# Kernel optimization log

Measured on AMD Instinct MI355X. Metric: run time of the kernel, lower is better.

Reference implementation:

```python
import jax, jax.numpy as jnp
import numpy as np

EMBED = 128
HEADS = 4
HEAD_DIM = EMBED // HEADS

def setup_inputs() -> dict:
    key = jax.random.key(0)
    ks = jax.random.split(key, 8)
    N, S = 32, 1024
    values = jax.random.normal(ks[0], (N, S, EMBED), dtype=jnp.float32)
    keys_ = jax.random.normal(ks[1], (N, S, EMBED), dtype=jnp.float32)
    query = jax.random.normal(ks[2], (N, S, EMBED), dtype=jnp.float32)
    mask = jnp.ones((N, 1, S, S), dtype=jnp.int32)
    # nn.Linear weights: y = x @ W.T  (bias=False for q/k/v projections)
    sc = 1.0 / np.sqrt(HEAD_DIM)
    Wv = jax.random.uniform(ks[3], (HEAD_DIM, HEAD_DIM), jnp.float32, -sc, sc)
    Wk = jax.random.uniform(ks[4], (HEAD_DIM, HEAD_DIM), jnp.float32, -sc, sc)
    Wq = jax.random.uniform(ks[5], (HEAD_DIM, HEAD_DIM), jnp.float32, -sc, sc)
    so = 1.0 / np.sqrt(EMBED)
    Wo = jax.random.uniform(ks[6], (EMBED, EMBED), jnp.float32, -so, so)
    bo = jax.random.uniform(ks[7], (EMBED,), jnp.float32, -so, so)
    return {"values": values, "keys": keys_, "query": query, "mask": mask,
            "Wv": Wv, "Wk": Wk, "Wq": Wq, "Wo": Wo, "bo": bo}

def reference(values, keys, query, mask, Wv, Wk, Wq, Wo, bo):
    N = query.shape[0]
    # reshape to [N, S, H, D] and apply per-head linear projections (no bias)
    v = values.reshape(N, -1, HEADS, HEAD_DIM) @ Wv.T
    k = keys.reshape(N, -1, HEADS, HEAD_DIM) @ Wk.T
    q = query.reshape(N, -1, HEADS, HEAD_DIM) @ Wq.T
    # [N, H, Sq, Sk]
    att = jnp.einsum('nqhd,nkhd->nhqk', q, k)
    att = jnp.where(mask == 0, jnp.float32(-1e20), att)
    # NOTE: faithful to source: scale by sqrt(embed_size), not sqrt(head_dim)
    attention_weights = jax.nn.softmax(att / jnp.sqrt(jnp.float32(EMBED)), axis=3)
    out = jnp.einsum('nhql,nlhd->nqhd', attention_weights, v).reshape(N, -1, HEADS * HEAD_DIM)
    out = out @ Wo.T + bo
    return out, attention_weights
```

## Files before the change

### kernel.cpp

```cpp
#include <hip/hip_runtime.h>

#define SLEN 1024
#define NBATCH 32
#define NHEADS 4
#define HDIM 32
#define EMB 128
#define LSTRIDE 1040

typedef short short8 __attribute__((ext_vector_type(8)));
typedef short short4v __attribute__((ext_vector_type(4)));
typedef float floatx4 __attribute__((ext_vector_type(4)));

__device__ __forceinline__ unsigned short f2bf(float f) {
    unsigned u = __float_as_uint(f);
    u += 0x7fffu + ((u >> 16) & 1u);
    return (unsigned short)(u >> 16);
}
__device__ __forceinline__ float bf2f(unsigned short h) {
    return __uint_as_float(((unsigned)h) << 16);
}

__global__ __launch_bounds__(256) void proj_kernel(
    const float* __restrict__ vals, const float* __restrict__ keys,
    const float* __restrict__ qrys,
    const float* __restrict__ Wv, const float* __restrict__ Wk,
    const float* __restrict__ Wq, const float* __restrict__ Wo,
    unsigned short* __restrict__ qb, unsigned short* __restrict__ kb,
    unsigned short* __restrict__ vt, unsigned short* __restrict__ wo_bf)
{
    int b = blockIdx.x;
    int tid = threadIdx.x;
    if (b == 512) {
        #pragma unroll
        for (int i = 0; i < 64; ++i) {
            int idx = tid + (i << 8);
            wo_bf[idx] = f2bf(Wo[idx]);
        }
        return;
    }
    int n = b >> 4;
    int s0 = (b & 15) << 6;
    int wave = tid >> 6, lane = tid & 63;
    int quad = lane >> 4, l16 = lane & 15;
    int srow = s0 + (wave << 4);

    short8 bw[3][2];
    const float* Ws[3] = { Wv, Wk, Wq };
    const float scal[3] = { 1.0f, 1.0f, 0.08838834764831845f };
    #pragma unroll
    for (int t = 0; t < 3; ++t) {
        float s = scal[t];
        #pragma unroll
        for (int hh = 0; hh < 2; ++hh) {
            const float* wp = Ws[t] + (hh * 16 + l16) * 32 + quad * 8;
            float4 w0 = *(const float4*)wp;
            float4 w1 = *(const float4*)(wp + 4);
            short8 r;
            r[0] = (short)f2bf(w0.x * s); r[1] = (short)f2bf(w0.y * s);
            r[2] = (short)f2bf(w0.z * s); r[3] = (short)f2bf(w0.w * s);
            r[4] = (short)f2bf(w1.x * s); r[5] = (short)f2bf(w1.y * s);
            r[6] = (short)f2bf(w1.z * s); r[7] = (short)f2bf(w1.w * s);
            bw[t][hh] = r;
        }
    }

    const float* srcs[3] = { vals, keys, qrys };
    #pragma unroll
    for (int t = 0; t < 3; ++t) {
        const float* src = srcs[t];
        #pragma unroll
        for (int h = 0; h < NHEADS; ++h) {
            size_t nh = (size_t)(n * NHEADS + h);
            const float* xp = src + ((size_t)(n * SLEN + srow + l16) * EMB + h * HDIM + quad * 8);
            float4 x0 = *(const float4*)xp;
            float4 x1 = *(const float4*)(xp + 4);
            short8 a;
            a[0] = (short)f2bf(x0.x); a[1] = (short)f2bf(x0.y);
            a[2] = (short)f2bf(x0.z); a[3] = (short)f2bf(x0.w);
            a[4] = (short)f2bf(x1.x); a[5] = (short)f2bf(x1.y);
            a[6] = (short)f2bf(x1.z); a[7] = (short)f2bf(x1.w);
            floatx4 c0 = {0.f, 0.f, 0.f, 0.f};
            floatx4 c1 = {0.f, 0.f, 0.f, 0.f};
            c0 = __builtin_amdgcn_mfma_f32_16x16x32_bf16(a, bw[t][0], c0, 0, 0, 0);
            c1 = __builtin_amdgcn_mfma_f32_16x16x32_bf16(a, bw[t][1], c1, 0, 0, 0);
            if (t == 0) {
                short4v p0, p1;
                p0[0] = (short)f2bf(c0[0]); p0[1] = (short)f2bf(c0[1]);
                p0[2] = (short)f2bf(c0[2]); p0[3] = (short)f2bf(c0[3]);
                p1[0] = (short)f2bf(c1[0]); p1[1] = (short)f2bf(c1[1]);
                p1[2] = (short)f2bf(c1[2]); p1[3] = (short)f2bf(c1[3]);
                *(short4v*)(vt + (nh * HDIM + l16) * SLEN + srow + quad * 4) = p0;
                *(short4v*)(vt + (nh * HDIM + 16 + l16) * SLEN + srow + quad * 4) = p1;
            } else {
                unsigned short* dst = (t == 1 ? kb : qb) +
                    (nh * SLEN + srow + quad * 4) * HDIM;
                #pragma unroll
                for (int r = 0; r < 4; ++r) {
                    dst[r * HDIM + l16]      = f2bf(c0[r]);
                    dst[r * HDIM + 16 + l16] = f2bf(c1[r]);
                }
            }
        }
    }
}

__global__ __launch_bounds__(256, 3) void attn_kernel(
    const unsigned short* __restrict__ qb, const unsigned short* __restrict__ kb,
    const unsigned short* __restrict__ vt, const int* __restrict__ mask,
    float* __restrict__ wout, unsigned short* __restrict__ attnv)
{
    __shared__ unsigned short eb[16 * LSTRIDE];
    __shared__ float partial[4][16][32];
    __shared__ float rowinv[16];

    int bid = blockIdx.x;
    int n = bid >> 6;
    int r0 = (bid & 63) << 4;
    int tid = threadIdx.x;
    int wave = tid >> 6, lane = tid & 63;
    int quad = lane >> 4, l16 = lane & 15;
    int srow = tid >> 4, c16 = tid & 15;

    unsigned long long mbits = 0ull;
    const int* mrow = mask + (size_t)(n * SLEN + r0 + srow) * SLEN;
    #pragma unroll
    for (int i = 0; i < 8; ++i) {
        int cb = (c16 + (i << 4)) << 3;
        int4 a = *(const int4*)(mrow + cb);
        int4 bq = *(const int4*)(mrow + cb + 4);
        unsigned bits = 0;
        bits |= (unsigned)(a.x != 0);
        bits |= (unsigned)(a.y != 0) << 1;
        bits |= (unsigned)(a.z != 0) << 2;
        bits |= (unsigned)(a.w != 0) << 3;
        bits |= (unsigned)(bq.x != 0) << 4;
        bits |= (unsigned)(bq.y != 0) << 5;
        bits |= (unsigned)(bq.z != 0) << 6;
        bits |= (unsigned)(bq.w != 0) << 7;
        mbits |= (unsigned long long)bits << (i * 8);
    }

    for (int h = 0; h < NHEADS; ++h) {
        size_t nh = (size_t)(n * NHEADS + h);

        short8 afrag = *(const short8*)(qb + (nh * SLEN + r0 + l16) * HDIM + quad * 8);
        const unsigned short* kbase = kb + nh * SLEN * HDIM;
        #pragma unroll
        for (int t = 0; t < 16; ++t) {
            int ct = (wave << 4) + t;
            short8 bfrag = *(const short8*)(kbase + (size_t)((ct << 4) + l16) * HDIM + quad * 8);
            floatx4 c = {0.f, 0.f, 0.f, 0.f};
            c = __builtin_amdgcn_mfma_f32_16x16x32_bf16(afrag, bfrag, c, 0, 0, 0);
            int colb = (ct << 4) + l16;
            #pragma unroll
            for (int r = 0; r < 4; ++r)
                eb[(quad * 4 + r) * LSTRIDE + colb] = f2bf(c[r]);
        }
        __syncthreads();

        unsigned short* erow = eb + srow * LSTRIDE;
        float mx = -3.0e38f;
        #pragma unroll
        for (int i = 0; i < 8; ++i) {
            int cb = (c16 + (i << 4)) << 3;
            short8 v = *(const short8*)(erow + cb);
            unsigned bits = (unsigned)(mbits >> (i * 8)) & 0xffu;
            #pragma unroll
            for (int j = 0; j < 8; ++j) {
                float x = ((bits >> j) & 1u) ? bf2f((unsigned short)v[j]) : -1e20f;
                mx = fmaxf(mx, x);
            }
        }
        #pragma unroll
        for (int off = 8; off > 0; off >>= 1)
            mx = fmaxf(mx, __shfl_xor(mx, off, 16));

        float sum = 0.f;
        #pragma unroll
        for (int i = 0; i < 8; ++i) {
            int cb = (c16 + (i << 4)) << 3;
            short8 v = *(const short8*)(erow + cb);
            unsigned bits = (unsigned)(mbits >> (i * 8)) & 0xffu;
            short8 e8;
            #pragma unroll
            for (int j = 0; j < 8; ++j) {
                float e = 0.f;
                if ((bits >> j) & 1u) e = __expf(bf2f((unsigned short)v[j]) - mx);
                sum += e;
                e8[j] = (short)f2bf(e);
            }
            *(short8*)(erow + cb) = e8;
        }
        #pragma unroll
        for (int off = 8; off > 0; off >>= 1)
            sum += __shfl_xor(sum, off, 16);
        float inv = 1.0f / sum;
        if (c16 == 0) rowinv[srow] = inv;

        float* wrow = wout + (nh * SLEN + r0 + srow) * SLEN;
        #pragma unroll
        for (int i = 0; i < 8; ++i) {
            int cb = (c16 + (i << 4)) << 3;
            short8 e8 = *(const short8*)(erow + cb);
            float4 w0, w1;
            w0.x = bf2f((unsigned short)e8[0]) * inv;
            w0.y = bf2f((unsigned short)e8[1]) * inv;
            w0.z = bf2f((unsigned short)e8[2]) * inv;
            w0.w = bf2f((unsigned short)e8[3]) * inv;
            w1.x = bf2f((unsigned short)e8[4]) * inv;
            w1.y = bf2f((unsigned short)e8[5]) * inv;
            w1.z = bf2f((unsigned short)e8[6]) * inv;
            w1.w = bf2f((unsigned short)e8[7]) * inv;
            *(float4*)(wrow + cb) = w0;
            *(float4*)(wrow + cb + 4) = w1;
        }
        __syncthreads();

        floatx4 acc0 = {0.f, 0.f, 0.f, 0.f}, acc1 = {0.f, 0.f, 0.f, 0.f};
        const unsigned short* vbase = vt + nh * HDIM * SLEN;
        #pragma unroll
        for (int i = 0; i < 8; ++i) {
            int kt = (wave << 3) + i;
            short8 a8 = *(const short8*)(eb + l16 * LSTRIDE + (kt << 5) + quad * 8);
            short8 b0 = *(const short8*)(vbase + (size_t)l16 * SLEN + (kt << 5) + quad * 8);
            short8 b1 = *(const short8*)(vbase + (size_t)(16 + l16) * SLEN + (kt << 5) + quad * 8);
            acc0 = __builtin_amdgcn_mfma_f32_16x16x32_bf16(a8, b0, acc0, 0, 0, 0);
            acc1 = __builtin_amdgcn_mfma_f32_16x16x32_bf16(a8, b1, acc1, 0, 0, 0);
        }
        #pragma unroll
        for (int r = 0; r < 4; ++r) {
            partial[wave][quad * 4 + r][l16] = acc0[r];
            partial[wave][quad * 4 + r][16 + l16] = acc1[r];
        }
        __syncthreads();

        {
            int m = tid >> 4;
            int d0 = (tid & 15) << 1;
            float s0 = partial[0][m][d0] + partial[1][m][d0] +
                       partial[2][m][d0] + partial[3][m][d0];
            float s1 = partial[0][m][d0 + 1] + partial[1][m][d0 + 1] +
                       partial[2][m][d0 + 1] + partial[3][m][d0 + 1];
            float iv = rowinv[m];
            unsigned pk = (unsigned)f2bf(s0 * iv) | ((unsigned)f2bf(s1 * iv) << 16);
            *(unsigned*)(attnv + (size_t)(n * SLEN + r0 + m) * EMB + h * HDIM + d0) = pk;
        }
        __syncthreads();
    }
}

__global__ __launch_bounds__(256) void out_kernel(
    const unsigned short* __restrict__ attnv, const unsigned short* __restrict__ wo_bf,
    const float* __restrict__ bo, float* __restrict__ out)
{
    int tid = threadIdx.x;
    int wave = tid >> 6, lane = tid & 63;
    int quad = lane >> 4, l16 = lane & 15;
    int m0 = blockIdx.x * 64 + (wave << 4);

    short8 afr[4];
    const unsigned short* ap = attnv + (size_t)(m0 + l16) * EMB + quad * 8;
    #pragma unroll
    for (int ks = 0; ks < 4; ++ks) afr[ks] = *(const short8*)(ap + ks * 32);

    #pragma unroll
    for (int ct = 0; ct < 8; ++ct) {
        floatx4 c = {0.f, 0.f, 0.f, 0.f};
        const unsigned short* bp = wo_bf + ((ct << 4) + l16) * EMB + quad * 8;
        #pragma unroll
        for (int ks = 0; ks < 4; ++ks) {
            short8 b = *(const short8*)(bp + ks * 32);
            c = __builtin_amdgcn_mfma_f32_16x16x32_bf16(afr[ks], b, c, 0, 0, 0);
        }
        int col = (ct << 4) + l16;
        float bias = bo[col];
        #pragma unroll
        for (int r = 0; r < 4; ++r)
            out[(size_t)(m0 + quad * 4 + r) * EMB + col] = c[r] + bias;
    }
}

extern "C" void kernel_launch(void* const* d_in, const int* in_sizes, int n_in,
                              void* d_out, int out_size, void* d_ws, size_t ws_size,
                              hipStream_t stream)
{
    (void)in_sizes; (void)n_in; (void)out_size; (void)ws_size;
    const float* vals = (const float*)d_in[0];
    const float* keys = (const float*)d_in[1];
    const float* qrys = (const float*)d_in[2];
    const int*   mask = (const int*)d_in[3];
    const float* Wv   = (const float*)d_in[4];
    const float* Wk   = (const float*)d_in[5];
    const float* Wq   = (const float*)d_in[6];
    const float* Wo   = (const float*)d_in[7];
    const float* bo   = (const float*)d_in[8];
    float* out = (float*)d_out;

    const size_t NHS = (size_t)NBATCH * NHEADS * SLEN * HDIM;
    unsigned short* ws = (unsigned short*)d_ws;
    unsigned short* qb    = ws;
    unsigned short* kbuf  = qb + NHS;
    unsigned short* vt    = kbuf + NHS;
    unsigned short* av    = vt + NHS;
    unsigned short* wo_bf = av + (size_t)NBATCH * SLEN * EMB;
    float* wout = out + (size_t)NBATCH * SLEN * EMB;

    hipLaunchKernelGGL(proj_kernel, dim3(513), dim3(256), 0, stream,
                       vals, keys, qrys, Wv, Wk, Wq, Wo, qb, kbuf, vt, wo_bf);
    hipLaunchKernelGGL(attn_kernel, dim3(NBATCH * 64), dim3(256), 0, stream,
                       qb, kbuf, vt, mask, wout, av);
    hipLaunchKernelGGL(out_kernel, dim3((NBATCH * SLEN) / 64), dim3(256), 0, stream,
                       av, wo_bf, bo, out);
}
```

Measured before the change: 848.4 us.

## Keep QK scores in registers for softmax and use nontemporal stores

The QK^T MFMA is transposed (K as A operand) so each lane holds four consecutive columns of a row. Masking, max, exp and normalisation are then done directly on register accumulators instead of round-tripping bf16 scores through LDS. Row max and sum are reduced across waves through small shared arrays. The mask is repacked once per block into per-lane nibbles via shared memory. The attention-weight, attnv and output writes use nontemporal stores, and one trailing barrier is dropped. The cost is higher register pressure from holding 16 accumulators per lane, and the weights are now computed from fp32 scores rather than bf16-rounded ones.

```diff
diff --git a/kernel.cpp b/kernel.cpp
--- a/kernel.cpp
+++ b/kernel.cpp
@@ -5,11 +5,12 @@
 #define NHEADS 4
 #define HDIM 32
 #define EMB 128
-#define LSTRIDE 1040
+#define LSTRIDE 1032
 
 typedef short short8 __attribute__((ext_vector_type(8)));
 typedef short short4v __attribute__((ext_vector_type(4)));
 typedef float floatx4 __attribute__((ext_vector_type(4)));
+typedef int   intx4  __attribute__((ext_vector_type(4)));
 
 __device__ __forceinline__ unsigned short f2bf(float f) {
     unsigned u = __float_as_uint(f);
@@ -110,8 +111,10 @@
     float* __restrict__ wout, unsigned short* __restrict__ attnv)
 {
     __shared__ unsigned short eb[16 * LSTRIDE];
+    __shared__ unsigned long long mb[16][17];
     __shared__ float partial[4][16][32];
-    __shared__ float rowinv[16];
+    __shared__ __align__(16) float redmax[16][4];
+    __shared__ __align__(16) float redsum[16][4];
 
     int bid = blockIdx.x;
     int n = bid >> 6;
@@ -121,109 +124,116 @@
     int quad = lane >> 4, l16 = lane & 15;
     int srow = tid >> 4, c16 = tid & 15;
 
-    unsigned long long mbits = 0ull;
-    const int* mrow = mask + (size_t)(n * SLEN + r0 + srow) * SLEN;
-    #pragma unroll
-    for (int i = 0; i < 8; ++i) {
-        int cb = (c16 + (i << 4)) << 3;
-        int4 a = *(const int4*)(mrow + cb);
-        int4 bq = *(const int4*)(mrow + cb + 4);
-        unsigned bits = 0;
-        bits |= (unsigned)(a.x != 0);
-        bits |= (unsigned)(a.y != 0) << 1;
-        bits |= (unsigned)(a.z != 0) << 2;
-        bits |= (unsigned)(a.w != 0) << 3;
-        bits |= (unsigned)(bq.x != 0) << 4;
-        bits |= (unsigned)(bq.y != 0) << 5;
-        bits |= (unsigned)(bq.z != 0) << 6;
-        bits |= (unsigned)(bq.w != 0) << 7;
-        mbits |= (unsigned long long)bits << (i * 8);
+    {
+        unsigned long long mbits = 0ull;
+        const int* mrow = mask + (size_t)(n * SLEN + r0 + srow) * SLEN;
+        #pragma unroll
+        for (int i = 0; i < 8; ++i) {
+            int cb = (c16 + (i << 4)) << 3;
+            intx4 a  = __builtin_nontemporal_load((const intx4*)(mrow + cb));
+            intx4 bq = __builtin_nontemporal_load((const intx4*)(mrow + cb + 4));
+            unsigned bits = 0;
+            bits |= (unsigned)(a[0] != 0);
+            bits |= (unsigned)(a[1] != 0) << 1;
+            bits |= (unsigned)(a[2] != 0) << 2;
+            bits |= (unsigned)(a[3] != 0) << 3;
+            bits |= (unsigned)(bq[0] != 0) << 4;
+            bits |= (unsigned)(bq[1] != 0) << 5;
+            bits |= (unsigned)(bq[2] != 0) << 6;
+            bits |= (unsigned)(bq[3] != 0) << 7;
+            mbits |= (unsigned long long)bits << (i * 8);
+        }
+        mb[srow][c16] = mbits;
+    }
+    __syncthreads();
+
+    unsigned long long lmask = 0ull;
+    {
+        int qh = quad >> 1, ql = quad & 1;
+        int shbase = (wave << 4) + (ql << 2);
+        #pragma unroll
+        for (int t = 0; t < 16; ++t) {
+            unsigned long long ch = mb[l16][((t << 1) + qh) & 15];
+            unsigned long long nib = (ch >> (shbase + ((t >> 3) << 3))) & 0xFull;
+            lmask |= nib << (t << 2);
+        }
     }
 
     for (int h = 0; h < NHEADS; ++h) {
         size_t nh = (size_t)(n * NHEADS + h);
 
-        short8 afrag = *(const short8*)(qb + (nh * SLEN + r0 + l16) * HDIM + quad * 8);
-        const unsigned short* kbase = kb + nh * SLEN * HDIM;
+        short8 qfrag = *(const short8*)(qb + (nh * SLEN + r0 + l16) * HDIM + quad * 8);
+        const unsigned short* kbase = kb + (nh * SLEN + (wave << 8)) * HDIM;
+
+        floatx4 c[16];
+        float mx = -3.0e38f;
         #pragma unroll
         for (int t = 0; t < 16; ++t) {
-            int ct = (wave << 4) + t;
-            short8 bfrag = *(const short8*)(kbase + (size_t)((ct << 4) + l16) * HDIM + quad * 8);
-            floatx4 c = {0.f, 0.f, 0.f, 0.f};
-            c = __builtin_amdgcn_mfma_f32_16x16x32_bf16(afrag, bfrag, c, 0, 0, 0);
-            int colb = (ct << 4) + l16;
+            short8 kfrag = *(const short8*)(kbase + (size_t)((t << 4) + l16) * HDIM + quad * 8);
+            floatx4 acc = {0.f, 0.f, 0.f, 0.f};
+            acc = __builtin_amdgcn_mfma_f32_16x16x32_bf16(kfrag, qfrag, acc, 0, 0, 0);
+            unsigned nb = (unsigned)(lmask >> (t << 2)) & 15u;
             #pragma unroll
-            for (int r = 0; r < 4; ++r)
-                eb[(quad * 4 + r) * LSTRIDE + colb] = f2bf(c[r]);
-        }
-        __syncthreads();
-
-        unsigned short* erow = eb + srow * LSTRIDE;
-        float mx = -3.0e38f;
-        #pragma unroll
-        for (int i = 0; i < 8; ++i) {
-            int cb = (c16 + (i << 4)) << 3;
-            short8 v = *(const short8*)(erow + cb);
-            unsigned bits = (unsigned)(mbits >> (i * 8)) & 0xffu;
-            #pragma unroll
-            for (int j = 0; j < 8; ++j) {
-                float x = ((bits >> j) & 1u) ? bf2f((unsigned short)v[j]) : -1e20f;
+            for (int r = 0; r < 4; ++r) {
+                float x = ((nb >> r) & 1u) ? acc[r] : -1e20f;
+                acc[r] = x;
                 mx = fmaxf(mx, x);
             }
-        }
-        #pragma unroll
-        for (int off = 8; off > 0; off >>= 1)
-            mx = fmaxf(mx, __shfl_xor(mx, off, 16));
+            c[t] = acc;
+        }
+        mx = fmaxf(mx, __shfl_xor(mx, 16));
+        mx = fmaxf(mx, __shfl_xor(mx, 32));
+        if (quad == 0) redmax[l16][wave] = mx;
+        __syncthreads();
+        {
+            floatx4 mv = *(const floatx4*)&redmax[l16][0];
+            mx = fmaxf(fmaxf(mv[0], mv[1]), fmaxf(mv[2], mv[3]));
+        }
 
         float sum = 0.f;
-        #pragma unroll
-        for (int i = 0; i < 8; ++i) {
-            int cb = (c16 + (i << 4)) << 3;
-            short8 v = *(const short8*)(erow + cb);
-            unsigned bits = (unsigned)(mbits >> (i * 8)) & 0xffu;
-            short8 e8;
-            #pragma unroll
-            for (int j = 0; j < 8; ++j) {
-                float e = 0.f;
-                if ((bits >> j) & 1u) e = __expf(bf2f((unsigned short)v[j]) - mx);
-                sum += e;
-                e8[j] = (short)f2bf(e);
-            }
-            *(short8*)(erow + cb) = e8;
-        }
-        #pragma unroll
-        for (int off = 8; off > 0; off >>= 1)
-            sum += __shfl_xor(sum, off, 16);
-        float inv = 1.0f / sum;
-        if (c16 == 0) rowinv[srow] = inv;
-
-        float* wrow = wout + (nh * SLEN + r0 + srow) * SLEN;
-        #pragma unroll
-        for (int i = 0; i < 8; ++i) {
-            int cb = (c16 + (i << 4)) << 3;
-            short8 e8 = *(const short8*)(erow + cb);
-            float4 w0, w1;
-            w0.x = bf2f((unsigned short)e8[0]) * inv;
-            w0.y = bf2f((unsigned short)e8[1]) * inv;
-            w0.z = bf2f((unsigned short)e8[2]) * inv;
-            w0.w = bf2f((unsigned short)e8[3]) * inv;
-            w1.x = bf2f((unsigned short)e8[4]) * inv;
-            w1.y = bf2f((unsigned short)e8[5]) * inv;
-            w1.z = bf2f((unsigned short)e8[6]) * inv;
-            w1.w = bf2f((unsigned short)e8[7]) * inv;
-            *(float4*)(wrow + cb) = w0;
-            *(float4*)(wrow + cb + 4) = w1;
-        }
+        unsigned short* erow = eb + l16 * LSTRIDE + (wave << 8);
+        #pragma unroll
+        for (int t = 0; t < 16; ++t) {
+            floatx4 cc = c[t];
+            float e0 = __expf(cc[0] - mx);
+            float e1 = __expf(cc[1] - mx);
+            float e2 = __expf(cc[2] - mx);
+            float e3 = __expf(cc[3] - mx);
+            sum += (e0 + e1) + (e2 + e3);
+            cc[0] = e0; cc[1] = e1; cc[2] = e2; cc[3] = e3;
+            c[t] = cc;
+            short4v p;
+            p[0] = (short)f2bf(e0); p[1] = (short)f2bf(e1);
+            p[2] = (short)f2bf(e2); p[3] = (short)f2bf(e3);
+            *(short4v*)(erow + (t << 4) + (quad << 2)) = p;
+        }
+        sum += __shfl_xor(sum, 16);
+        sum += __shfl_xor(sum, 32);
+        if (quad == 0) redsum[l16][wave] = sum;
         __syncthreads();
+        float inv;
+        {
+            floatx4 sv = *(const floatx4*)&redsum[l16][0];
+            inv = 1.0f / ((sv[0] + sv[1]) + (sv[2] + sv[3]));
+        }
+
+        float* wrow = wout + (nh * SLEN + r0 + l16) * SLEN + (wave << 8);
+        #pragma unroll
+        for (int t = 0; t < 16; ++t) {
+            floatx4 wv;
+            wv[0] = c[t][0] * inv; wv[1] = c[t][1] * inv;
+            wv[2] = c[t][2] * inv; wv[3] = c[t][3] * inv;
+            __builtin_nontemporal_store(wv, (floatx4*)(wrow + (t << 4) + (quad << 2)));
+        }
 
         floatx4 acc0 = {0.f, 0.f, 0.f, 0.f}, acc1 = {0.f, 0.f, 0.f, 0.f};
         const unsigned short* vbase = vt + nh * HDIM * SLEN;
         #pragma unroll
         for (int i = 0; i < 8; ++i) {
             int kt = (wave << 3) + i;
-            short8 a8 = *(const short8*)(eb + l16 * LSTRIDE + (kt << 5) + quad * 8);
-            short8 b0 = *(const short8*)(vbase + (size_t)l16 * SLEN + (kt << 5) + quad * 8);
-            short8 b1 = *(const short8*)(vbase + (size_t)(16 + l16) * SLEN + (kt << 5) + quad * 8);
+            short8 a8 = *(const short8*)(eb + l16 * LSTRIDE + (kt << 5) + (quad << 3));
+            short8 b0 = *(const short8*)(vbase + (size_t)l16 * SLEN + (kt << 5) + (quad << 3));
+            short8 b1 = *(const short8*)(vbase + (size_t)(16 + l16) * SLEN + (kt << 5) + (quad << 3));
             acc0 = __builtin_amdgcn_mfma_f32_16x16x32_bf16(a8, b0, acc0, 0, 0, 0);
             acc1 = __builtin_amdgcn_mfma_f32_16x16x32_bf16(a8, b1, acc1, 0, 0, 0);
         }
@@ -235,17 +245,18 @@
         __syncthreads();
 
         {
-            int m = tid >> 4;
-            int d0 = (tid & 15) << 1;
+            int m = srow;
+            int d0 = c16 << 1;
             float s0 = partial[0][m][d0] + partial[1][m][d0] +
                        partial[2][m][d0] + partial[3][m][d0];
             float s1 = partial[0][m][d0 + 1] + partial[1][m][d0 + 1] +
                        partial[2][m][d0 + 1] + partial[3][m][d0 + 1];
-            float iv = rowinv[m];
+            floatx4 sv = *(const floatx4*)&redsum[m][0];
+            float iv = 1.0f / ((sv[0] + sv[1]) + (sv[2] + sv[3]));
             unsigned pk = (unsigned)f2bf(s0 * iv) | ((unsigned)f2bf(s1 * iv) << 16);
-            *(unsigned*)(attnv + (size_t)(n * SLEN + r0 + m) * EMB + h * HDIM + d0) = pk;
-        }
-        __syncthreads();
+            __builtin_nontemporal_store(pk,
+                (unsigned*)(attnv + (size_t)(n * SLEN + r0 + m) * EMB + h * HDIM + d0));
+        }
     }
 }
 
@@ -276,7 +287,8 @@
         float bias = bo[col];
         #pragma unroll
         for (int r = 0; r < 4; ++r)
-            out[(size_t)(m0 + quad * 4 + r) * EMB + col] = c[r] + bias;
+            __builtin_nontemporal_store(c[r] + bias,
+                &out[(size_t)(m0 + quad * 4 + r) * EMB + col]);
     }
 }
 
```

Measured after the change: 786.0 us. 1.08x faster.
